# Performance work log

Hardware: AMD Instinct MI355X
Metric: run time of the kernel (lower is better)

## Reference

```python
import jax, jax.numpy as jnp
import numpy as np


def setup_inputs() -> dict:
    key = jax.random.key(0)
    ks = jax.random.split(key, 5)
    B, S, D, L = 16, 256, 768, 32
    return {
        "head": jax.random.normal(ks[0], (B, S, D), dtype=jnp.float32),
        "dep": jax.random.normal(ks[1], (B, S, D), dtype=jnp.float32),
        "label_U_diag": jax.random.normal(ks[2], (L, D), dtype=jnp.float32) * 0.02,
        "label_W": jax.random.normal(ks[3], (L, 2 * D), dtype=jnp.float32) * 0.02,
        "label_b": jax.random.normal(ks[4], (L,), dtype=jnp.float32) * 0.02,
    }


def reference(head, dep, label_U_diag, label_W, label_b):
    # head, dep: [b, s, d]; label_U_diag: [l, d]; label_W: [l, 2d]; label_b: [l]
    d = head.shape[-1]
    # Bilinear term with diagonal U: t1[b,l,i,o] = sum_d head[b,i,d]*U[l,d]*dep[b,o,d]
    t1 = jnp.einsum('bid,ld,bod->blio', head, label_U_diag, dep)
    # Linear term: W @ concat(head_i, dep_o) = W_h @ head_i + W_d @ dep_o
    W_h, W_d = label_W[:, :d], label_W[:, d:]
    t2_h = jnp.einsum('ld,bid->bli', W_h, head)  # [b, l, s]
    t2_d = jnp.einsum('ld,bod->blo', W_d, dep)   # [b, l, s]
    return t1 + t2_h[:, :, :, None] + t2_d[:, :, None, :] + label_b[None, :, None, None]
```

## Files before the change

kernel.cpp:

```cpp
#include <hip/hip_runtime.h>
#include <hip/hip_bf16.h>
#include <stdint.h>


#define B_ 16
#define S_ 256
#define D_ 768
#define L_ 32

typedef unsigned short ushort_t;
typedef __attribute__((ext_vector_type(4))) float f32x4;
typedef __attribute__((ext_vector_type(8))) short s16x8;

typedef __attribute__((address_space(1))) const unsigned int guint;
typedef __attribute__((address_space(3))) unsigned int luint;

__device__ __forceinline__ void async_load16(const ushort_t* g, ushort_t* l) {
  __builtin_amdgcn_global_load_lds((guint*)g, (luint*)l, 16, 0, 0);
}

__device__ __forceinline__ unsigned int pack_bf16(float f0, float f1) {
  unsigned int u0 = __builtin_bit_cast(unsigned int, f0) + 0x8000u;
  unsigned int u1 = __builtin_bit_cast(unsigned int, f1) + 0x8000u;
  return __builtin_amdgcn_perm(u1, u0, 0x07060302);
}

__global__ __launch_bounds__(256) void prep_kernel(
    const float* __restrict__ head, const float* __restrict__ dep,
    const float* __restrict__ labelW, ushort_t* __restrict__ depb,
    float* __restrict__ t2h, float* __restrict__ t2d) {
  const int wave = threadIdx.x >> 6;
  const int lane = threadIdx.x & 63;
  const int g = blockIdx.x * 4 + wave;
  const int sel = g >> 10;
  const int idx = g & 1023;
  const int b = idx >> 6;
  const int row0 = (idx & 63) * 4;
  const float* src = sel ? dep : head;
  float* t2x = sel ? t2d : t2h;
  const int d0 = lane * 12;

  float h[4][12];
  const float* rp = src + ((size_t)(b * S_ + row0)) * D_ + d0;
#pragma unroll
  for (int r = 0; r < 4; ++r) {
    float4 v0 = *(const float4*)(rp + (size_t)r * D_);
    float4 v1 = *(const float4*)(rp + (size_t)r * D_ + 4);
    float4 v2 = *(const float4*)(rp + (size_t)r * D_ + 8);
    h[r][0] = v0.x; h[r][1] = v0.y; h[r][2] = v0.z; h[r][3] = v0.w;
    h[r][4] = v1.x; h[r][5] = v1.y; h[r][6] = v1.z; h[r][7] = v1.w;
    h[r][8] = v2.x; h[r][9] = v2.y; h[r][10] = v2.z; h[r][11] = v2.w;
  }
  if (sel) {
#pragma unroll
    for (int r = 0; r < 4; ++r) {
      uint2 q0 = {pack_bf16(h[r][0], h[r][1]), pack_bf16(h[r][2], h[r][3])};
      uint2 q1 = {pack_bf16(h[r][4], h[r][5]), pack_bf16(h[r][6], h[r][7])};
      uint2 q2 = {pack_bf16(h[r][8], h[r][9]), pack_bf16(h[r][10], h[r][11])};
      uint2* dp = (uint2*)(depb + ((size_t)(b * S_ + row0 + r)) * D_ + d0);
      dp[0] = q0; dp[1] = q1; dp[2] = q2;
    }
  }
  const float* wbase = labelW + sel * D_ + d0;
  for (int l = 0; l < L_; ++l) {
    const float* wp = wbase + (size_t)l * (2 * D_);
    float4 w0 = *(const float4*)(wp);
    float4 w1 = *(const float4*)(wp + 4);
    float4 w2 = *(const float4*)(wp + 8);
    float w[12] = {w0.x, w0.y, w0.z, w0.w, w1.x, w1.y, w1.z, w1.w,
                   w2.x, w2.y, w2.z, w2.w};
    float p0 = 0.f, p1 = 0.f, p2 = 0.f, p3 = 0.f;
#pragma unroll
    for (int j = 0; j < 12; ++j) {
      p0 += h[0][j] * w[j];
      p1 += h[1][j] * w[j];
      p2 += h[2][j] * w[j];
      p3 += h[3][j] * w[j];
    }
#pragma unroll
    for (int off = 32; off >= 1; off >>= 1) {
      p0 += __shfl_xor(p0, off);
      p1 += __shfl_xor(p1, off);
      p2 += __shfl_xor(p2, off);
      p3 += __shfl_xor(p3, off);
    }
    if (lane < 4) {
      float v = lane == 0 ? p0 : lane == 1 ? p1 : lane == 2 ? p2 : p3;
      t2x[((size_t)(b * L_ + l)) * S_ + row0 + lane] = v;
    }
  }
}

__global__ __launch_bounds__(256, 2) void main_kernel(
    const float* __restrict__ head, const ushort_t* __restrict__ depb,
    const float* __restrict__ U, const float* __restrict__ bias,
    const float* __restrict__ t2h, const float* __restrict__ t2d,
    float* __restrict__ out) {
  __shared__ ushort_t As[128 * 32];
  __shared__ ushort_t Bs[256 * 32];
  __shared__ float T2[384];

  const int bid = blockIdx.x;
  const int ic = bid & 1;
  const int bl = bid >> 1;
  const int l = bl & (L_ - 1);
  const int b = bl >> 5;
  const int ti = ic * 128;
  const int t = threadIdx.x;
  const int lane = t & 63;
  const int wave = t >> 6;
  const int m_base = (wave >> 1) * 64;
  const int n_base = (wave & 1) * 128;

  for (int i = t; i < 384; i += 256)
    T2[i] = (i < 128) ? t2h[((size_t)(b * L_ + l)) * S_ + ti + i]
                      : t2d[((size_t)(b * L_ + l)) * S_ + (i - 128)];
  const float bv = bias[l];

  const int row0 = t >> 2;
  const int kq = (t & 3) * 8;
  const float* hp0 = head + ((size_t)(b * S_ + ti + row0)) * D_ + kq;
  const float* hp1 = hp0 + (size_t)64 * D_;
  const float* Up = U + (size_t)l * D_ + kq;
  const ushort_t* dp = depb + ((size_t)(b * S_ + row0)) * D_ + kq;
  ushort_t* asw0 = As + t * 8;
  ushort_t* asw1 = As + t * 8 + 2048;

  f32x4 acc[4][8];
#pragma unroll
  for (int i = 0; i < 4; ++i)
#pragma unroll
    for (int j = 0; j < 8; ++j) acc[i][j] = {0.f, 0.f, 0.f, 0.f};

  const ushort_t* ar = As + ((m_base + (lane & 15)) * 32 + (lane >> 4) * 8);
  const ushort_t* br = Bs + ((n_base + (lane & 15)) * 32 + (lane >> 4) * 8);

  for (int kk = 0; kk < D_; kk += 32) {
    __syncthreads();
#pragma unroll
    for (int j = 0; j < 4; ++j)
      async_load16(dp + kk + (size_t)j * 64 * D_, Bs + j * 2048 + t * 8);
    float4 h0 = *(const float4*)(hp0 + kk);
    float4 h1 = *(const float4*)(hp0 + kk + 4);
    float4 h2 = *(const float4*)(hp1 + kk);
    float4 h3 = *(const float4*)(hp1 + kk + 4);
    float4 u0 = *(const float4*)(Up + kk);
    float4 u1 = *(const float4*)(Up + kk + 4);
    uint4 w0, w1;
    w0.x = pack_bf16(h0.x * u0.x, h0.y * u0.y);
    w0.y = pack_bf16(h0.z * u0.z, h0.w * u0.w);
    w0.z = pack_bf16(h1.x * u1.x, h1.y * u1.y);
    w0.w = pack_bf16(h1.z * u1.z, h1.w * u1.w);
    w1.x = pack_bf16(h2.x * u0.x, h2.y * u0.y);
    w1.y = pack_bf16(h2.z * u0.z, h2.w * u0.w);
    w1.z = pack_bf16(h3.x * u1.x, h3.y * u1.y);
    w1.w = pack_bf16(h3.z * u1.z, h3.w * u1.w);
    *(uint4*)asw0 = w0;
    *(uint4*)asw1 = w1;
    __syncthreads();

    s16x8 af[4], bf[8];
#pragma unroll
    for (int rt = 0; rt < 4; ++rt) af[rt] = *(const s16x8*)(ar + rt * 512);
#pragma unroll
    for (int ct = 0; ct < 8; ++ct) bf[ct] = *(const s16x8*)(br + ct * 512);
#pragma unroll
    for (int rt = 0; rt < 4; ++rt)
#pragma unroll
      for (int ct = 0; ct < 8; ++ct)
        acc[rt][ct] = __builtin_amdgcn_mfma_f32_16x16x32_bf16(af[rt], bf[ct],
                                                              acc[rt][ct], 0, 0, 0);
  }

  const int colg = lane & 15;
  const int rgrp = lane >> 4;
  float* ob = out + (((size_t)(b * L_ + l)) * S_ + ti) * S_;
#pragma unroll
  for (int rt = 0; rt < 4; ++rt) {
    const int r0 = m_base + rt * 16 + rgrp * 4;
#pragma unroll
    for (int ct = 0; ct < 8; ++ct) {
      const int c = n_base + ct * 16 + colg;
      const float addc = T2[128 + c] + bv;
      float* p = ob + (size_t)r0 * S_ + c;
#pragma unroll
      for (int r = 0; r < 4; ++r)
        p[(size_t)r * S_] = acc[rt][ct][r] + T2[r0 + r] + addc;
    }
  }
}

extern "C" void kernel_launch(void* const* d_in, const int* in_sizes, int n_in,
                              void* d_out, int out_size, void* d_ws, size_t ws_size,
                              hipStream_t stream) {
  const float* head = (const float*)d_in[0];
  const float* dep = (const float*)d_in[1];
  const float* U = (const float*)d_in[2];
  const float* W = (const float*)d_in[3];
  const float* bias = (const float*)d_in[4];
  float* out = (float*)d_out;

  ushort_t* depb = (ushort_t*)d_ws;
  float* t2h = (float*)((char*)d_ws + (size_t)B_ * S_ * D_ * 2);
  float* t2d = t2h + (size_t)B_ * L_ * S_;

  prep_kernel<<<512, 256, 0, stream>>>(head, dep, W, depb, t2h, t2d);
  main_kernel<<<B_ * L_ * 2, 256, 0, stream>>>(head, depb, U, bias, t2h, t2d, out);
}
```

Measured before the change: 249.9 us.

## Double-buffer LDS tiles, pre-tile dep layout, swizzle block order, nontemporal output stores

The main GEMM loop now double-buffers the A and B LDS tiles. The next k-slice's async DMA and head loads are issued before the current MFMA compute, which cuts one barrier per iteration and hides global latency. The prep kernel writes bf16 dep in a k-group-major tiled layout, so each DMA chunk is contiguous and the LDS fragment reads become stride-free (fewer bank conflicts). The grid is also remapped so consecutive hardware blocks spread across batch/label, and output stores use nontemporal hints. LDS use doubles, which may limit occupancy at 2 blocks per CU.

```diff
diff --git a/kernel.cpp b/kernel.cpp
--- a/kernel.cpp
+++ b/kernel.cpp
@@ -7,6 +7,7 @@
 #define S_ 256
 #define D_ 768
 #define L_ 32
+#define KQ_ (D_ / 8)
 
 typedef unsigned short ushort_t;
 typedef __attribute__((ext_vector_type(4))) float f32x4;
@@ -52,13 +53,28 @@
     h[r][8] = v2.x; h[r][9] = v2.y; h[r][10] = v2.z; h[r][11] = v2.w;
   }
   if (sel) {
+    const size_t bb = (size_t)b * (KQ_ * S_ * 8);
+    const int m = lane >> 1;
 #pragma unroll
     for (int r = 0; r < 4; ++r) {
-      uint2 q0 = {pack_bf16(h[r][0], h[r][1]), pack_bf16(h[r][2], h[r][3])};
-      uint2 q1 = {pack_bf16(h[r][4], h[r][5]), pack_bf16(h[r][6], h[r][7])};
-      uint2 q2 = {pack_bf16(h[r][8], h[r][9]), pack_bf16(h[r][10], h[r][11])};
-      uint2* dp = (uint2*)(depb + ((size_t)(b * S_ + row0 + r)) * D_ + d0);
-      dp[0] = q0; dp[1] = q1; dp[2] = q2;
+      const int col = row0 + r;
+      unsigned int q0 = pack_bf16(h[r][0], h[r][1]);
+      unsigned int q1 = pack_bf16(h[r][2], h[r][3]);
+      unsigned int q2 = pack_bf16(h[r][4], h[r][5]);
+      unsigned int q3 = pack_bf16(h[r][6], h[r][7]);
+      unsigned int q4 = pack_bf16(h[r][8], h[r][9]);
+      unsigned int q5 = pack_bf16(h[r][10], h[r][11]);
+      if ((lane & 1) == 0) {
+        uint4 a = {q0, q1, q2, q3};
+        uint2 c = {q4, q5};
+        *(uint4*)(depb + bb + ((size_t)(3 * m) * S_ + col) * 8) = a;
+        *(uint2*)(depb + bb + ((size_t)(3 * m + 1) * S_ + col) * 8) = c;
+      } else {
+        uint2 c = {q0, q1};
+        uint4 a = {q2, q3, q4, q5};
+        *(uint2*)(depb + bb + ((size_t)(3 * m + 1) * S_ + col) * 8 + 4) = c;
+        *(uint4*)(depb + bb + ((size_t)(3 * m + 2) * S_ + col) * 8) = a;
+      }
     }
   }
   const float* wbase = labelW + sel * D_ + d0;
@@ -96,11 +112,12 @@
     const float* __restrict__ U, const float* __restrict__ bias,
     const float* __restrict__ t2h, const float* __restrict__ t2d,
     float* __restrict__ out) {
-  __shared__ ushort_t As[128 * 32];
-  __shared__ ushort_t Bs[256 * 32];
+  __shared__ __attribute__((aligned(16))) ushort_t As[2 * 128 * 32];
+  __shared__ __attribute__((aligned(16))) ushort_t Bs[2 * 256 * 32];
   __shared__ float T2[384];
 
-  const int bid = blockIdx.x;
+  const int hw = blockIdx.x;
+  const int bid = ((hw & 7) << 7) | (hw >> 3);
   const int ic = bid & 1;
   const int bl = bid >> 1;
   const int l = bl & (L_ - 1);
@@ -118,13 +135,14 @@
   const float bv = bias[l];
 
   const int row0 = t >> 2;
-  const int kq = (t & 3) * 8;
-  const float* hp0 = head + ((size_t)(b * S_ + ti + row0)) * D_ + kq;
+  const int kg = t & 3;
+  const float* hp0 = head + ((size_t)(b * S_ + ti + row0)) * D_ + kg * 8;
   const float* hp1 = hp0 + (size_t)64 * D_;
-  const float* Up = U + (size_t)l * D_ + kq;
-  const ushort_t* dp = depb + ((size_t)(b * S_ + row0)) * D_ + kq;
-  ushort_t* asw0 = As + t * 8;
-  ushort_t* asw1 = As + t * 8 + 2048;
+  const float* Up = U + (size_t)l * D_ + kg * 8;
+  const ushort_t* dpb = depb + (size_t)b * (KQ_ * S_ * 8);
+  const int awo0 = (kg * 128 + row0) * 8;
+  const int awo1 = awo0 + 64 * 8;
+  const int dmo = t * 8;
 
   f32x4 acc[4][8];
 #pragma unroll
@@ -132,45 +150,83 @@
 #pragma unroll
     for (int j = 0; j < 8; ++j) acc[i][j] = {0.f, 0.f, 0.f, 0.f};
 
-  const ushort_t* ar = As + ((m_base + (lane & 15)) * 32 + (lane >> 4) * 8);
-  const ushort_t* br = Bs + ((n_base + (lane & 15)) * 32 + (lane >> 4) * 8);
-
-  for (int kk = 0; kk < D_; kk += 32) {
+  const int aro = ((lane >> 4) * 128 + m_base + (lane & 15)) * 8;
+  const int bro = ((lane >> 4) * 256 + n_base + (lane & 15)) * 8;
+
+#define DMA_B(BUF, KK)                                                       \
+  {                                                                          \
+    ushort_t* bw = Bs + (BUF) * 8192;                                        \
+    const ushort_t* gs = dpb + (size_t)(KK) * 256;                           \
+    async_load16(gs + dmo, bw + dmo);                                        \
+    async_load16(gs + 2048 + dmo, bw + 2048 + dmo);                          \
+    async_load16(gs + 4096 + dmo, bw + 4096 + dmo);                          \
+    async_load16(gs + 6144 + dmo, bw + 6144 + dmo);                          \
+  }
+
+#define PACK_WRITE_A(BUF)                                                    \
+  {                                                                          \
+    uint4 w0, w1;                                                            \
+    w0.x = pack_bf16(h0.x * u0.x, h0.y * u0.y);                              \
+    w0.y = pack_bf16(h0.z * u0.z, h0.w * u0.w);                              \
+    w0.z = pack_bf16(h1.x * u1.x, h1.y * u1.y);                              \
+    w0.w = pack_bf16(h1.z * u1.z, h1.w * u1.w);                              \
+    w1.x = pack_bf16(h2.x * u0.x, h2.y * u0.y);                              \
+    w1.y = pack_bf16(h2.z * u0.z, h2.w * u0.w);                              \
+    w1.z = pack_bf16(h3.x * u1.x, h3.y * u1.y);                              \
+    w1.w = pack_bf16(h3.z * u1.z, h3.w * u1.w);                              \
+    ushort_t* aw = As + (BUF) * 4096;                                        \
+    *(uint4*)(aw + awo0) = w0;                                               \
+    *(uint4*)(aw + awo1) = w1;                                               \
+  }
+
+#define COMPUTE(CUR)                                                         \
+  {                                                                          \
+    const ushort_t* ar = As + (CUR) * 4096 + aro;                            \
+    const ushort_t* br = Bs + (CUR) * 8192 + bro;                            \
+    s16x8 af[4], bf[8];                                                      \
+    _Pragma("unroll") for (int rt = 0; rt < 4; ++rt)                         \
+        af[rt] = *(const s16x8*)(ar + rt * 128);                             \
+    _Pragma("unroll") for (int ct = 0; ct < 8; ++ct)                         \
+        bf[ct] = *(const s16x8*)(br + ct * 128);                             \
+    _Pragma("unroll") for (int rt = 0; rt < 4; ++rt)                         \
+      _Pragma("unroll") for (int ct = 0; ct < 8; ++ct)                       \
+          acc[rt][ct] = __builtin_amdgcn_mfma_f32_16x16x32_bf16(             \
+              af[rt], bf[ct], acc[rt][ct], 0, 0, 0);                         \
+  }
+
+  {
+    DMA_B(0, 0);
+    float4 h0 = *(const float4*)(hp0);
+    float4 h1 = *(const float4*)(hp0 + 4);
+    float4 h2 = *(const float4*)(hp1);
+    float4 h3 = *(const float4*)(hp1 + 4);
+    float4 u0 = *(const float4*)(Up);
+    float4 u1 = *(const float4*)(Up + 4);
+    PACK_WRITE_A(0);
+  }
+  __syncthreads();
+
+  int cur = 0;
+  for (int kk = 0; kk < D_ - 32; kk += 32) {
+    DMA_B(cur ^ 1, kk + 32);
+    float4 h0 = *(const float4*)(hp0 + kk + 32);
+    float4 h1 = *(const float4*)(hp0 + kk + 36);
+    float4 h2 = *(const float4*)(hp1 + kk + 32);
+    float4 h3 = *(const float4*)(hp1 + kk + 36);
+    float4 u0 = *(const float4*)(Up + kk + 32);
+    float4 u1 = *(const float4*)(Up + kk + 36);
+
+    COMPUTE(cur);
+
+    PACK_WRITE_A(cur ^ 1);
     __syncthreads();
-#pragma unroll
-    for (int j = 0; j < 4; ++j)
-      async_load16(dp + kk + (size_t)j * 64 * D_, Bs + j * 2048 + t * 8);
-    float4 h0 = *(const float4*)(hp0 + kk);
-    float4 h1 = *(const float4*)(hp0 + kk + 4);
-    float4 h2 = *(const float4*)(hp1 + kk);
-    float4 h3 = *(const float4*)(hp1 + kk + 4);
-    float4 u0 = *(const float4*)(Up + kk);
-    float4 u1 = *(const float4*)(Up + kk + 4);
-    uint4 w0, w1;
-    w0.x = pack_bf16(h0.x * u0.x, h0.y * u0.y);
-    w0.y = pack_bf16(h0.z * u0.z, h0.w * u0.w);
-    w0.z = pack_bf16(h1.x * u1.x, h1.y * u1.y);
-    w0.w = pack_bf16(h1.z * u1.z, h1.w * u1.w);
-    w1.x = pack_bf16(h2.x * u0.x, h2.y * u0.y);
-    w1.y = pack_bf16(h2.z * u0.z, h2.w * u0.w);
-    w1.z = pack_bf16(h3.x * u1.x, h3.y * u1.y);
-    w1.w = pack_bf16(h3.z * u1.z, h3.w * u1.w);
-    *(uint4*)asw0 = w0;
-    *(uint4*)asw1 = w1;
-    __syncthreads();
-
-    s16x8 af[4], bf[8];
-#pragma unroll
-    for (int rt = 0; rt < 4; ++rt) af[rt] = *(const s16x8*)(ar + rt * 512);
-#pragma unroll
-    for (int ct = 0; ct < 8; ++ct) bf[ct] = *(const s16x8*)(br + ct * 512);
-#pragma unroll
-    for (int rt = 0; rt < 4; ++rt)
-#pragma unroll
-      for (int ct = 0; ct < 8; ++ct)
-        acc[rt][ct] = __builtin_amdgcn_mfma_f32_16x16x32_bf16(af[rt], bf[ct],
-                                                              acc[rt][ct], 0, 0, 0);
-  }
+    cur ^= 1;
+  }
+  COMPUTE(cur);
+
+#undef DMA_B
+#undef PACK_WRITE_A
+#undef COMPUTE
 
   const int colg = lane & 15;
   const int rgrp = lane >> 4;
@@ -185,7 +241,8 @@
       float* p = ob + (size_t)r0 * S_ + c;
 #pragma unroll
       for (int r = 0; r < 4; ++r)
-        p[(size_t)r * S_] = acc[rt][ct][r] + T2[r0 + r] + addc;
+        __builtin_nontemporal_store(acc[rt][ct][r] + T2[r0 + r] + addc,
+                                    p + (size_t)r * S_);
     }
   }
 }
```

Result: slower. 268.0 us (+7.2%).

## Pre-tile dep into MFMA fragment layout, double-buffer A in LDS, load B directly

Applied to the files above, without the earlier changes.

The prep kernel now writes bf16 dep in a k-group-major tiled layout, so each main-kernel lane can load its MFMA B fragments straight from global memory into registers, dropping the LDS staging of B. The A tile (head*U) is double-buffered in swizzled LDS, and the next tile's global loads are issued before the current MFMAs, leaving one barrier per k-step. Each wave now covers all 128 rows by 64 columns, and block IDs are remapped to change scheduling order. The cost is more register pressure from two sets of B fragments and redundant global reads of B fragments across waves.

```diff
diff --git a/kernel.cpp b/kernel.cpp
--- a/kernel.cpp
+++ b/kernel.cpp
@@ -7,17 +7,12 @@
 #define S_ 256
 #define D_ 768
 #define L_ 32
+#define KQ_ (D_ / 8)
+#define NT_ 24
 
 typedef unsigned short ushort_t;
 typedef __attribute__((ext_vector_type(4))) float f32x4;
 typedef __attribute__((ext_vector_type(8))) short s16x8;
-
-typedef __attribute__((address_space(1))) const unsigned int guint;
-typedef __attribute__((address_space(3))) unsigned int luint;
-
-__device__ __forceinline__ void async_load16(const ushort_t* g, ushort_t* l) {
-  __builtin_amdgcn_global_load_lds((guint*)g, (luint*)l, 16, 0, 0);
-}
 
 __device__ __forceinline__ unsigned int pack_bf16(float f0, float f1) {
   unsigned int u0 = __builtin_bit_cast(unsigned int, f0) + 0x8000u;
@@ -52,13 +47,28 @@
     h[r][8] = v2.x; h[r][9] = v2.y; h[r][10] = v2.z; h[r][11] = v2.w;
   }
   if (sel) {
+    const size_t bb = (size_t)b * (KQ_ * S_ * 8);
+    const int m = lane >> 1;
 #pragma unroll
     for (int r = 0; r < 4; ++r) {
-      uint2 q0 = {pack_bf16(h[r][0], h[r][1]), pack_bf16(h[r][2], h[r][3])};
-      uint2 q1 = {pack_bf16(h[r][4], h[r][5]), pack_bf16(h[r][6], h[r][7])};
-      uint2 q2 = {pack_bf16(h[r][8], h[r][9]), pack_bf16(h[r][10], h[r][11])};
-      uint2* dp = (uint2*)(depb + ((size_t)(b * S_ + row0 + r)) * D_ + d0);
-      dp[0] = q0; dp[1] = q1; dp[2] = q2;
+      const int col = row0 + r;
+      unsigned int q0 = pack_bf16(h[r][0], h[r][1]);
+      unsigned int q1 = pack_bf16(h[r][2], h[r][3]);
+      unsigned int q2 = pack_bf16(h[r][4], h[r][5]);
+      unsigned int q3 = pack_bf16(h[r][6], h[r][7]);
+      unsigned int q4 = pack_bf16(h[r][8], h[r][9]);
+      unsigned int q5 = pack_bf16(h[r][10], h[r][11]);
+      if ((lane & 1) == 0) {
+        uint4 a = {q0, q1, q2, q3};
+        uint2 c = {q4, q5};
+        *(uint4*)(depb + bb + ((size_t)(3 * m) * S_ + col) * 8) = a;
+        *(uint2*)(depb + bb + ((size_t)(3 * m + 1) * S_ + col) * 8) = c;
+      } else {
+        uint2 c = {q0, q1};
+        uint4 a = {q2, q3, q4, q5};
+        *(uint2*)(depb + bb + ((size_t)(3 * m + 1) * S_ + col) * 8 + 4) = c;
+        *(uint4*)(depb + bb + ((size_t)(3 * m + 2) * S_ + col) * 8) = a;
+      }
     }
   }
   const float* wbase = labelW + sel * D_ + d0;
@@ -91,16 +101,19 @@
   }
 }
 
+
+#define SWZ(o) ((o) ^ ((((o) >> 10) & 3) << 4))
+
 __global__ __launch_bounds__(256, 2) void main_kernel(
     const float* __restrict__ head, const ushort_t* __restrict__ depb,
     const float* __restrict__ U, const float* __restrict__ bias,
     const float* __restrict__ t2h, const float* __restrict__ t2d,
     float* __restrict__ out) {
-  __shared__ ushort_t As[128 * 32];
-  __shared__ ushort_t Bs[256 * 32];
+  __shared__ __attribute__((aligned(16))) ushort_t As[2 * 128 * 32];
   __shared__ float T2[384];
 
-  const int bid = blockIdx.x;
+  const int hw = blockIdx.x;
+  const int bid = ((hw & 7) << 7) | (hw >> 3);
   const int ic = bid & 1;
   const int bl = bid >> 1;
   const int l = bl & (L_ - 1);
@@ -109,8 +122,6 @@
   const int t = threadIdx.x;
   const int lane = t & 63;
   const int wave = t >> 6;
-  const int m_base = (wave >> 1) * 64;
-  const int n_base = (wave & 1) * 128;
 
   for (int i = t; i < 384; i += 256)
     T2[i] = (i < 128) ? t2h[((size_t)(b * L_ + l)) * S_ + ti + i]
@@ -118,34 +129,33 @@
   const float bv = bias[l];
 
   const int row0 = t >> 2;
-  const int kq = (t & 3) * 8;
-  const float* hp0 = head + ((size_t)(b * S_ + ti + row0)) * D_ + kq;
+  const int kg = t & 3;
+  const float* hp0 = head + ((size_t)(b * S_ + ti + row0)) * D_ + kg * 8;
   const float* hp1 = hp0 + (size_t)64 * D_;
-  const float* Up = U + (size_t)l * D_ + kq;
-  const ushort_t* dp = depb + ((size_t)(b * S_ + row0)) * D_ + kq;
-  ushort_t* asw0 = As + t * 8;
-  ushort_t* asw1 = As + t * 8 + 2048;
-
-  f32x4 acc[4][8];
-#pragma unroll
-  for (int i = 0; i < 4; ++i)
-#pragma unroll
-    for (int j = 0; j < 8; ++j) acc[i][j] = {0.f, 0.f, 0.f, 0.f};
-
-  const ushort_t* ar = As + ((m_base + (lane & 15)) * 32 + (lane >> 4) * 8);
-  const ushort_t* br = Bs + ((n_base + (lane & 15)) * 32 + (lane >> 4) * 8);
-
-  for (int kk = 0; kk < D_; kk += 32) {
-    __syncthreads();
-#pragma unroll
-    for (int j = 0; j < 4; ++j)
-      async_load16(dp + kk + (size_t)j * 64 * D_, Bs + j * 2048 + t * 8);
-    float4 h0 = *(const float4*)(hp0 + kk);
-    float4 h1 = *(const float4*)(hp0 + kk + 4);
-    float4 h2 = *(const float4*)(hp1 + kk);
-    float4 h3 = *(const float4*)(hp1 + kk + 4);
-    float4 u0 = *(const float4*)(Up + kk);
-    float4 u1 = *(const float4*)(Up + kk + 4);
+  const float* Up = U + (size_t)l * D_ + kg * 8;
+  const int awo0s = SWZ((kg * 128 + row0) * 8);
+  const int awo1s = awo0s + 512;
+
+  const int aros = SWZ(((lane >> 4) * 128 + (lane & 15)) * 8);
+
+  const ushort_t* dfb = depb + (size_t)b * (KQ_ * S_ * 8) +
+                        ((size_t)((lane >> 4) * 256 + wave * 64 + (lane & 15))) * 8;
+
+  f32x4 acc[8][4];
+#pragma unroll
+  for (int i = 0; i < 8; ++i)
+#pragma unroll
+    for (int j = 0; j < 4; ++j) acc[i][j] = {0.f, 0.f, 0.f, 0.f};
+
+  s16x8 bfA[4], bfB[4];
+
+  {
+    float4 h0 = *(const float4*)(hp0);
+    float4 h1 = *(const float4*)(hp0 + 4);
+    float4 h2 = *(const float4*)(hp1);
+    float4 h3 = *(const float4*)(hp1 + 4);
+    float4 u0 = *(const float4*)(Up);
+    float4 u1 = *(const float4*)(Up + 4);
     uint4 w0, w1;
     w0.x = pack_bf16(h0.x * u0.x, h0.y * u0.y);
     w0.y = pack_bf16(h0.z * u0.z, h0.w * u0.w);
@@ -155,32 +165,74 @@
     w1.y = pack_bf16(h2.z * u0.z, h2.w * u0.w);
     w1.z = pack_bf16(h3.x * u1.x, h3.y * u1.y);
     w1.w = pack_bf16(h3.z * u1.z, h3.w * u1.w);
-    *(uint4*)asw0 = w0;
-    *(uint4*)asw1 = w1;
-    __syncthreads();
-
-    s16x8 af[4], bf[8];
-#pragma unroll
-    for (int rt = 0; rt < 4; ++rt) af[rt] = *(const s16x8*)(ar + rt * 512);
-#pragma unroll
-    for (int ct = 0; ct < 8; ++ct) bf[ct] = *(const s16x8*)(br + ct * 512);
-#pragma unroll
-    for (int rt = 0; rt < 4; ++rt)
-#pragma unroll
-      for (int ct = 0; ct < 8; ++ct)
-        acc[rt][ct] = __builtin_amdgcn_mfma_f32_16x16x32_bf16(af[rt], bf[ct],
-                                                              acc[rt][ct], 0, 0, 0);
-  }
+    *(uint4*)(As + awo0s) = w0;
+    *(uint4*)(As + awo1s) = w1;
+#pragma unroll
+    for (int ct = 0; ct < 4; ++ct)
+      bfA[ct] = *(const s16x8*)(dfb + ct * 128);
+  }
+  asm volatile("s_waitcnt lgkmcnt(0)" ::: "memory");
+  __builtin_amdgcn_s_barrier();
+  __builtin_amdgcn_sched_barrier(0);
+
+#define ITER(PB, BFC, BFN, tcur)                                              \
+  {                                                                           \
+    int tn = (tcur) + 1;                                                      \
+    if (tn == NT_) tn = 0;     \
+    const float* hA = hp0 + tn * 32;                                          \
+    const float* hB = hp1 + tn * 32;                                          \
+    const float* uA = Up + tn * 32;                                           \
+    float4 h0 = *(const float4*)(hA);                                         \
+    float4 h1 = *(const float4*)(hA + 4);                                     \
+    float4 h2 = *(const float4*)(hB);                                         \
+    float4 h3 = *(const float4*)(hB + 4);                                     \
+    float4 u0 = *(const float4*)(uA);                                         \
+    float4 u1 = *(const float4*)(uA + 4);                                     \
+    const ushort_t* dfn = dfb + (size_t)tn * 8192;                            \
+    _Pragma("unroll") for (int ct = 0; ct < 4; ++ct)                          \
+        BFN[ct] = *(const s16x8*)(dfn + ct * 128);                            \
+    __builtin_amdgcn_sched_barrier(0);       \
+    s16x8 af[8];                                                              \
+    _Pragma("unroll") for (int rt = 0; rt < 8; ++rt)                          \
+        af[rt] = *(const s16x8*)(As + (PB)*4096 + aros + rt * 128);           \
+    __builtin_amdgcn_s_setprio(1);                                            \
+    _Pragma("unroll") for (int rt = 0; rt < 8; ++rt)                          \
+      _Pragma("unroll") for (int ct = 0; ct < 4; ++ct)                        \
+          acc[rt][ct] = __builtin_amdgcn_mfma_f32_16x16x32_bf16(              \
+              af[rt], BFC[ct], acc[rt][ct], 0, 0, 0);                         \
+    __builtin_amdgcn_s_setprio(0);                                            \
+    uint4 w0, w1;                                                             \
+    w0.x = pack_bf16(h0.x * u0.x, h0.y * u0.y);                               \
+    w0.y = pack_bf16(h0.z * u0.z, h0.w * u0.w);                               \
+    w0.z = pack_bf16(h1.x * u1.x, h1.y * u1.y);                               \
+    w0.w = pack_bf16(h1.z * u1.z, h1.w * u1.w);                               \
+    w1.x = pack_bf16(h2.x * u0.x, h2.y * u0.y);                               \
+    w1.y = pack_bf16(h2.z * u0.z, h2.w * u0.w);                               \
+    w1.z = pack_bf16(h3.x * u1.x, h3.y * u1.y);                               \
+    w1.w = pack_bf16(h3.z * u1.z, h3.w * u1.w);                               \
+    ushort_t* aw = As + ((PB) ^ 1) * 4096;                                    \
+    *(uint4*)(aw + awo0s) = w0;                                               \
+    *(uint4*)(aw + awo1s) = w1;                                               \
+    asm volatile("s_waitcnt lgkmcnt(0)" ::: "memory");                        \
+    __builtin_amdgcn_s_barrier();                                             \
+    __builtin_amdgcn_sched_barrier(0);                                        \
+  }
+
+  for (int tt = 0; tt < NT_; tt += 2) {
+    ITER(0, bfA, bfB, tt);
+    ITER(1, bfB, bfA, tt + 1);
+  }
+#undef ITER
 
   const int colg = lane & 15;
   const int rgrp = lane >> 4;
   float* ob = out + (((size_t)(b * L_ + l)) * S_ + ti) * S_;
 #pragma unroll
-  for (int rt = 0; rt < 4; ++rt) {
-    const int r0 = m_base + rt * 16 + rgrp * 4;
-#pragma unroll
-    for (int ct = 0; ct < 8; ++ct) {
-      const int c = n_base + ct * 16 + colg;
+  for (int rt = 0; rt < 8; ++rt) {
+    const int r0 = rt * 16 + rgrp * 4;
+#pragma unroll
+    for (int ct = 0; ct < 4; ++ct) {
+      const int c = wave * 64 + ct * 16 + colg;
       const float addc = T2[128 + c] + bv;
       float* p = ob + (size_t)r0 * S_ + c;
 #pragma unroll
```

Measured after the change: 229.5 us. 1.09x faster.
